# Kernel tuning notes

Hardware: AMD Instinct MI355X
Metric: run time of the kernel (lower is better)

## Reference

```python
import math
import jax, jax.numpy as jnp
import numpy as np

B, L, D, H = 256, 32, 512, 512
NEG_INF = -1e9


def setup_inputs() -> dict:
    key = jax.random.key(0)
    ks = jax.random.split(key, 7)
    x = jax.random.normal(ks[0], (B, L, D), dtype=jnp.float32)
    length = jax.random.randint(ks[1], (B,), 2, L + 1)  # valid lengths in [2, L]
    # word_linear: D -> 2H
    W_word = jax.random.normal(ks[2], (2 * H, D), dtype=jnp.float32) * (1.0 / math.sqrt(D))
    b_word = jnp.zeros((2 * H,), dtype=jnp.float32)
    # comp_linear: 2H -> 5H (orthogonal-ish init; scale is fine for a reference)
    W_comp = jax.random.normal(ks[3], (5 * H, 2 * H), dtype=jnp.float32) * (1.0 / math.sqrt(2 * H))
    b_comp = jnp.zeros((5 * H,), dtype=jnp.float32)
    comp_query = jax.random.normal(ks[4], (H,), dtype=jnp.float32) * 0.01
    return {"x": x, "length": length, "W_word": W_word, "b_word": b_word,
            "W_comp": W_comp, "b_comp": b_comp, "comp_query": comp_query}


def _treelstm_compose(hl, cl, hr, cr, W_comp, b_comp):
    # hl/hr: [B, n, H] -> parent h, c: [B, n, H]
    v = jnp.einsum('bnd,kd->bnk', jnp.concatenate([hl, hr], axis=2), W_comp) + b_comp
    i, fl, fr, u, o = jnp.split(v, 5, axis=2)
    c = cl * jax.nn.sigmoid(fl + 1.0) + cr * jax.nn.sigmoid(fr + 1.0) \
        + jnp.tanh(u) * jax.nn.sigmoid(i)
    h = jax.nn.sigmoid(o) * jnp.tanh(c)
    return h, c


def reference(x, length, W_word, b_word, W_comp, b_comp, comp_query):
    length_mask = (jnp.arange(L)[None, :] < length[:, None]).astype(jnp.float32)  # [B, L]
    # leaf states from word_linear (use_leaf_rnn=False path)
    hc = jnp.einsum('bld,kd->blk', x, W_word) + b_word  # [B, L, 2H]
    h, c = jnp.split(hc, 2, axis=2)
    scale = 1.0 / math.sqrt(H)
    for i in range(L - 1):
        new_h, new_c = _treelstm_compose(h[:, :-1], c[:, :-1], h[:, 1:], c[:, 1:], W_comp, b_comp)
        if i < L - 2:
            # eval-mode greedy composition selection (basic.greedy_select)
            logits = jnp.sum(comp_query * new_h, axis=-1) * scale  # [B, L-1-i]
            mask = length_mask[:, i + 1:]
            logits = jnp.where(mask > 0, logits, NEG_INF)
            select = jax.nn.one_hot(jnp.argmax(logits, axis=1), logits.shape[1], dtype=jnp.float32)
            cum = jnp.cumsum(select, axis=1)
            left = (1.0 - cum)[:, :, None]
            right = (cum - select)[:, :, None]
            sel = select[:, :, None]
            new_h = sel * new_h + left * h[:, :-1] + right * h[:, 1:]
            new_c = sel * new_c + left * c[:, :-1] + right * c[:, 1:]
        done = length_mask[:, i + 1][:, None, None]
        h = done * new_h + (1.0 - done) * h[:, :-1]
        c = done * new_c + (1.0 - done) * c[:, :-1]
    return h[:, 0, :]  # final root hidden state [B, H]
```

## Files before the change

### kernel.cpp

```cpp
#include <hip/hip_runtime.h>
#include <cmath>

#define B_   256
#define L_   32
#define H_   512
#define NH5  2560
#define N2   5120
#define SCALE 0.044194173824159216f

__device__ float g_h [B_*L_*H_];
__device__ float g_c [B_*L_*H_];
__device__ float g_al[(size_t)B_*L_*NH5];
__device__ float g_ar[(size_t)B_*L_*NH5];
__device__ float g_logit[B_*L_];
__device__ int   g_list[B_*L_];
__device__ int   g_count[B_];
__device__ int   g_merged[B_];
__device__ int   g_mpos[B_];
__device__ int   g_rows[B_*L_];
__device__ int   g_nrows;
__device__ int   g_mlist[2][B_];
__device__ int   g_cnt[2];

__device__ __forceinline__ float sigm(float x) { return 1.0f / (1.0f + expf(-x)); }

__device__ __forceinline__ void gate4(float* d, const float* __restrict__ a,
                                      const float* __restrict__ b,
                                      const float* __restrict__ bc, int off) {
  float4 x = *(const float4*)(a + off);
  float4 y = *(const float4*)(b + off);
  float4 z = *(const float4*)(bc + off);
  d[0]=x.x+y.x+z.x; d[1]=x.y+y.y+z.y; d[2]=x.z+y.z+z.z; d[3]=x.w+y.w+z.w;
}
__device__ __forceinline__ void gate2(float* d, const float* __restrict__ a,
                                      const float* __restrict__ b,
                                      const float* __restrict__ bc, int off) {
  float2 x = *(const float2*)(a + off);
  float2 y = *(const float2*)(b + off);
  float2 z = *(const float2*)(bc + off);
  d[0]=x.x+y.x+z.x; d[1]=x.y+y.y+z.y;
}

__global__ __launch_bounds__(256) void scan_init(const int* __restrict__ length) {
  __shared__ int sw[4];
  __shared__ int s_off[256];
  __shared__ int s_len[256];
  const int t = threadIdx.x;
  const int len = length[t];
  s_len[t] = len;
  int v = len;
#pragma unroll
  for (int off = 1; off < 64; off <<= 1) {
    int o = __shfl_up(v, off, 64);
    if ((t & 63) >= off) v += o;
  }
  if ((t & 63) == 63) sw[t >> 6] = v;
  __syncthreads();
  int base = 0;
  for (int w = 0; w < (t >> 6); w++) base += sw[w];
  const int incl = base + v;
  s_off[t] = incl - len;
  if (t == 255) g_nrows = incl;
  g_count[t] = len; g_merged[t] = -2; g_mpos[t] = 0;
  if (t == 0) { g_cnt[0] = 0; g_cnt[1] = 0; }
  __syncthreads();
  for (int idx = t; idx < B_*L_; idx += 256) {
    const int b = idx >> 5, s = idx & 31;
    g_list[idx] = s;
    if (s < s_len[b]) g_rows[s_off[b] + s] = idx;
  }
}

template<int MODE>
__global__ __launch_bounds__(512) void gemm_big(
    const float* __restrict__ Aext,
    const float* __restrict__ Bm,
    const float* __restrict__ bias)
{
  const int NR = g_nrows;
  const int m0 = blockIdx.y * 128;
  if (m0 >= NR) return;
  const int n0 = blockIdx.x * 128;

  const int tid = threadIdx.x;
  const int w = tid >> 6, l = tid & 63;
  const int tx = (w & 1) * 8 + (l & 7);
  const int ty = (w >> 1) * 8 + (l >> 3);

  __shared__ float As[8][128];
  __shared__ float Bs[8][128];

  const bool stgB = tid >= 256;
  const int st = tid & 255;
  const int rs = st >> 1, qs = (st & 1) * 4;

  const float* Abase = (MODE == 0) ? Aext : g_h;
  const float* sptr;
  if (!stgB) {
    int mr = m0 + rs; if (mr >= NR) mr = NR - 1;
    sptr = Abase + (size_t)g_rows[mr] * 512 + qs;
  } else {
    int nrow = n0 + rs;
    if (MODE == 0) sptr = Bm + (size_t)nrow * 512 + qs;
    else sptr = Bm + (nrow < NH5 ? (size_t)nrow * 1024
                                 : (size_t)(nrow - NH5) * 1024 + 512) + qs;
  }

  float4 sv = *(const float4*)(sptr);
  float acc[4][8] = {};

  for (int k0 = 0; k0 < 512; k0 += 8) {
    __syncthreads();
    if (!stgB) {
      As[qs+0][rs] = sv.x; As[qs+1][rs] = sv.y; As[qs+2][rs] = sv.z; As[qs+3][rs] = sv.w;
    } else {
      Bs[qs+0][rs] = sv.x; Bs[qs+1][rs] = sv.y; Bs[qs+2][rs] = sv.z; Bs[qs+3][rs] = sv.w;
    }
    __syncthreads();
    if (k0 + 8 < 512) sv = *(const float4*)(sptr + k0 + 8);
#pragma unroll
    for (int k = 0; k < 8; k++) {
      float4 a4 = *(const float4*)&As[k][ty*4];
      float af[4] = {a4.x, a4.y, a4.z, a4.w};
      float bf[8];
      float4 t0 = *(const float4*)&Bs[k][tx*8];
      float4 t1 = *(const float4*)&Bs[k][tx*8 + 4];
      bf[0]=t0.x; bf[1]=t0.y; bf[2]=t0.z; bf[3]=t0.w;
      bf[4]=t1.x; bf[5]=t1.y; bf[6]=t1.z; bf[7]=t1.w;
#pragma unroll
      for (int i = 0; i < 4; i++)
#pragma unroll
        for (int j = 0; j < 8; j++)
          acc[i][j] = fmaf(af[i], bf[j], acc[i][j]);
    }
  }

#pragma unroll
  for (int i = 0; i < 4; i++) {
    int mrow = m0 + ty*4 + i;
    if (mrow >= NR) continue;
    int crow = g_rows[mrow];
#pragma unroll
    for (int j = 0; j < 8; j++) {
      int n = n0 + tx*8 + j;
      float v = acc[i][j];
      if (MODE == 0) {
        v += bias[n];
        if (n < H_) g_h[(size_t)crow*H_ + n]        = v;
        else        g_c[(size_t)crow*H_ + (n - H_)] = v;
      } else {
        if (n < NH5) g_al[(size_t)crow*NH5 + n]         = v;
        else         g_ar[(size_t)crow*NH5 + (n - NH5)] = v;
      }
    }
  }
}

__global__ __launch_bounds__(256) void iter0_logits(const int* __restrict__ length,
                                                    const float* __restrict__ bc,
                                                    const float* __restrict__ qv) {
  __shared__ float sred[4];
  const int p = blockIdx.x, b = blockIdx.y;
  if (p >= length[b] - 1) return;
  const float* al = g_al + (size_t)(b*L_ + p)*NH5;
  const float* ar = g_ar + (size_t)(b*L_ + p + 1)*NH5;
  const float* cl = g_c  + (size_t)(b*L_ + p)*H_;
  const float* cr = g_c  + (size_t)(b*L_ + p + 1)*H_;
  const int j0 = threadIdx.x * 2;
  float vi[2], vfl[2], vfr[2], vu[2], vo[2];
  gate2(vi , al, ar, bc,        j0);
  gate2(vfl, al, ar, bc, H_   + j0);
  gate2(vfr, al, ar, bc, 2*H_ + j0);
  gate2(vu , al, ar, bc, 3*H_ + j0);
  gate2(vo , al, ar, bc, 4*H_ + j0);
  float2 CL = *(const float2*)(cl + j0);
  float2 CR = *(const float2*)(cr + j0);
  float2 Q  = *(const float2*)(qv + j0);
  const float clv[2] = {CL.x, CL.y};
  const float crv[2] = {CR.x, CR.y};
  const float qq [2] = {Q.x, Q.y};
  float part = 0.f;
#pragma unroll
  for (int u = 0; u < 2; ++u) {
    float c = clv[u]*sigm(vfl[u]+1.f) + crv[u]*sigm(vfr[u]+1.f) + tanhf(vu[u])*sigm(vi[u]);
    float h = sigm(vo[u])*tanhf(c);
    part = fmaf(qq[u], h, part);
  }
#pragma unroll
  for (int off = 32; off; off >>= 1) part += __shfl_down(part, off, 64);
  if ((threadIdx.x & 63) == 0) sred[threadIdx.x >> 6] = part;
  __syncthreads();
  if (threadIdx.x == 0)
    g_logit[b*L_ + p] = (sred[0]+sred[1]+sred[2]+sred[3]) * SCALE;
}

__global__ __launch_bounds__(512) void select_merge(int iter,
    const int* __restrict__ length,
    const float* __restrict__ bc,
    const float* __restrict__ qv,
    float* __restrict__ out)
{
  __shared__ float sred[4];
  __shared__ int s_sel[3];
  const int b = blockIdx.x, tid = threadIdx.x;
  const bool fin = (iter == L_-2);
  if (b == 0 && tid == 0) g_cnt[(iter & 1) ^ 1] = 0;

  const int m     = g_count[b];
  const int pslot = g_merged[b];
  const int ppos  = g_mpos[b];
  int* list = g_list + b*L_;

  if (iter > 0 && pslot >= 0) {
    const int half = tid >> 7, lt = tid & 127;
    int sl = -1, sr = -1;
    if (half == 0)      { if (ppos > 0)     { sl = list[ppos-1]; sr = list[ppos];   } }
    else if (half == 1) { if (ppos < m - 1) { sl = list[ppos];   sr = list[ppos+1]; } }
    float part = 0.f;
    if (sl >= 0) {
      const float* al = g_al + (size_t)(b*L_+sl)*NH5;
      const float* ar = g_ar + (size_t)(b*L_+sr)*NH5;
      const float* cl = g_c  + (size_t)(b*L_+sl)*H_;
      const float* cr = g_c  + (size_t)(b*L_+sr)*H_;
      const int j0 = lt * 4;
      float vi[4], vfl[4], vfr[4], vu[4], vo[4];
      gate4(vi , al, ar, bc,        j0);
      gate4(vfl, al, ar, bc, H_   + j0);
      gate4(vfr, al, ar, bc, 2*H_ + j0);
      gate4(vu , al, ar, bc, 3*H_ + j0);
      gate4(vo , al, ar, bc, 4*H_ + j0);
      float4 CL = *(const float4*)(cl + j0);
      float4 CR = *(const float4*)(cr + j0);
      float4 Q  = *(const float4*)(qv + j0);
      const float clv[4] = {CL.x,CL.y,CL.z,CL.w};
      const float crv[4] = {CR.x,CR.y,CR.z,CR.w};
      const float qq [4] = {Q.x,Q.y,Q.z,Q.w};
#pragma unroll
      for (int u = 0; u < 4; ++u) {
        float c = clv[u]*sigm(vfl[u]+1.f) + crv[u]*sigm(vfr[u]+1.f) + tanhf(vu[u])*sigm(vi[u]);
        float h = sigm(vo[u])*tanhf(c);
        part = fmaf(qq[u], h, part);
      }
    }
#pragma unroll
    for (int off = 32; off; off >>= 1) part += __shfl_down(part, off, 64);
    if ((tid & 63) == 0 && tid < 256) sred[tid >> 6] = part;
    __syncthreads();
    if (tid == 0   && ppos > 0)     g_logit[b*L_ + list[ppos-1]] = (sred[0]+sred[1])*SCALE;
    if (tid == 128 && ppos < m - 1) g_logit[b*L_ + list[ppos]]   = (sred[2]+sred[3])*SCALE;
  }

  const bool active = iter < (length[b] - 1);
  if (!active) {
    if (tid == 0) g_merged[b] = -1;
    if (fin)
      out[(size_t)b*H_ + tid] = g_h[(size_t)(b*L_)*H_ + tid];
    return;
  }

  __syncthreads();

  if (tid < 64) {
    float lg = -1e30f; int idx = tid;
    if (tid < m - 1) lg = g_logit[b*L_ + list[tid]];
#pragma unroll
    for (int off = 32; off; off >>= 1) {
      float olg = __shfl_down(lg, off, 64);
      int   oid = __shfl_down(idx, off, 64);
      if (olg > lg || (olg == lg && oid < idx)) { lg = olg; idx = oid; }
    }
    if (tid == 0) { s_sel[0] = idx; s_sel[1] = list[idx]; s_sel[2] = list[idx+1]; }
  }
  __syncthreads();
  const int pos = s_sel[0], sl = s_sel[1], sr = s_sel[2];

  {
    const float* al = g_al + (size_t)(b*L_+sl)*NH5;
    const float* ar = g_ar + (size_t)(b*L_+sr)*NH5;
    float*       cl = g_c  + (size_t)(b*L_+sl)*H_;
    const float* cr = g_c  + (size_t)(b*L_+sr)*H_;
    float*       hl = g_h  + (size_t)(b*L_+sl)*H_;
    const int j = tid;
    float vi  = al[j]       + ar[j]       + bc[j];
    float vfl = al[H_+j]    + ar[H_+j]    + bc[H_+j];
    float vfr = al[2*H_+j]  + ar[2*H_+j]  + bc[2*H_+j];
    float vu  = al[3*H_+j]  + ar[3*H_+j]  + bc[3*H_+j];
    float vo  = al[4*H_+j]  + ar[4*H_+j]  + bc[4*H_+j];
    float c = cl[j]*sigm(vfl+1.f) + cr[j]*sigm(vfr+1.f) + tanhf(vu)*sigm(vi);
    float h = sigm(vo)*tanhf(c);
    cl[j] = c; hl[j] = h;
    if (fin)
      out[(size_t)b*H_ + j] = h;
  }
  if (tid == 0) {
    for (int n = pos+1; n < m-1; n++) list[n] = list[n+1];
    g_count[b]  = m - 1;
    g_merged[b] = sl;
    g_mpos[b]   = pos;
    int k = atomicAdd(&g_cnt[iter & 1], 1);
    g_mlist[iter & 1][k] = b;
  }
}

__global__ __launch_bounds__(256) void gemm_iter(int par, const float* __restrict__ Wc)
{
  const int nact = g_cnt[par];
  const int m0 = blockIdx.y * 32;
  if (m0 >= nact) return;
  const int n0 = blockIdx.x * 64;
  const int tid = threadIdx.x;

  __shared__ float As[2][32][32];
  __shared__ float Bs[2][32][64];

  const int ra = tid >> 3, qa = (tid & 7) * 4;
  int mr = m0 + ra; if (mr >= nact) mr = nact - 1;
  const int bbA = g_mlist[par][mr];
  const float* aptr = g_h + (size_t)(bbA*L_ + g_merged[bbA]) * 512 + qa;

  const int rb = tid >> 2, qb = (tid & 3) * 8;
  const int nr = n0 + rb;
  const float* bptr = (nr < NH5) ? Wc + (size_t)nr * 1024 + qb
                                 : Wc + (size_t)(nr - NH5) * 1024 + 512 + qb;

  const int tx = tid & 15, ty = tid >> 4;

  float4 av  = *(const float4*)(aptr);
  float4 bv0 = *(const float4*)(bptr);
  float4 bv1 = *(const float4*)(bptr + 4);
  As[0][qa+0][ra]=av.x;  As[0][qa+1][ra]=av.y;  As[0][qa+2][ra]=av.z;  As[0][qa+3][ra]=av.w;
  Bs[0][qb+0][rb]=bv0.x; Bs[0][qb+1][rb]=bv0.y; Bs[0][qb+2][rb]=bv0.z; Bs[0][qb+3][rb]=bv0.w;
  Bs[0][qb+4][rb]=bv1.x; Bs[0][qb+5][rb]=bv1.y; Bs[0][qb+6][rb]=bv1.z; Bs[0][qb+7][rb]=bv1.w;
  __syncthreads();

  float acc[2][4] = {};
  for (int s = 0; s < 16; ++s) {
    const int cur = s & 1;
    if (s < 15) {
      const int ko = 32 * (s + 1);
      av  = *(const float4*)(aptr + ko);
      bv0 = *(const float4*)(bptr + ko);
      bv1 = *(const float4*)(bptr + ko + 4);
    }
#pragma unroll
    for (int k = 0; k < 32; k++) {
      float2 a2 = *(const float2*)&As[cur][k][ty*2];
      float4 b4 = *(const float4*)&Bs[cur][k][tx*4];
      acc[0][0] = fmaf(a2.x, b4.x, acc[0][0]);
      acc[0][1] = fmaf(a2.x, b4.y, acc[0][1]);
      acc[0][2] = fmaf(a2.x, b4.z, acc[0][2]);
      acc[0][3] = fmaf(a2.x, b4.w, acc[0][3]);
      acc[1][0] = fmaf(a2.y, b4.x, acc[1][0]);
      acc[1][1] = fmaf(a2.y, b4.y, acc[1][1]);
      acc[1][2] = fmaf(a2.y, b4.z, acc[1][2]);
      acc[1][3] = fmaf(a2.y, b4.w, acc[1][3]);
    }
    if (s < 15) {
      const int nx = cur ^ 1;
      As[nx][qa+0][ra]=av.x;  As[nx][qa+1][ra]=av.y;  As[nx][qa+2][ra]=av.z;  As[nx][qa+3][ra]=av.w;
      Bs[nx][qb+0][rb]=bv0.x; Bs[nx][qb+1][rb]=bv0.y; Bs[nx][qb+2][rb]=bv0.z; Bs[nx][qb+3][rb]=bv0.w;
      Bs[nx][qb+4][rb]=bv1.x; Bs[nx][qb+5][rb]=bv1.y; Bs[nx][qb+6][rb]=bv1.z; Bs[nx][qb+7][rb]=bv1.w;
      __syncthreads();
    }
  }

#pragma unroll
  for (int i = 0; i < 2; i++) {
    int mrow = m0 + ty*2 + i;
    if (mrow >= nact) continue;
    int bb = g_mlist[par][mrow];
    size_t base = (size_t)(bb*L_ + g_merged[bb]) * NH5;
    int n = n0 + tx*4;
    float4 v = make_float4(acc[i][0], acc[i][1], acc[i][2], acc[i][3]);
    if (n < NH5) *(float4*)(g_al + base + n)         = v;
    else         *(float4*)(g_ar + base + (n - NH5)) = v;
  }
}

extern "C" void kernel_launch(void* const* d_in, const int* in_sizes, int n_in,
                              void* d_out, int out_size, void* d_ws, size_t ws_size,
                              hipStream_t stream)
{
  (void)in_sizes; (void)n_in; (void)out_size; (void)d_ws; (void)ws_size;
  const float* x      = (const float*)d_in[0];
  const int*   length = (const int*)  d_in[1];
  const float* W_word = (const float*)d_in[2];
  const float* b_word = (const float*)d_in[3];
  const float* W_comp = (const float*)d_in[4];
  const float* b_comp = (const float*)d_in[5];
  const float* q      = (const float*)d_in[6];
  float* out = (float*)d_out;

  scan_init<<<1, 256, 0, stream>>>(length);

  gemm_big<0><<<dim3(1024/128, 64), 512, 0, stream>>>(x, W_word, b_word);
  gemm_big<1><<<dim3(N2/128,   64), 512, 0, stream>>>(nullptr, W_comp, nullptr);

  iter0_logits<<<dim3(L_-1, B_), 256, 0, stream>>>(length, b_comp, q);

  for (int i = 0; i < L_-1; i++) {
    select_merge<<<B_, 512, 0, stream>>>(i, length, b_comp, q, out);
    if (i < L_-2)
      gemm_iter<<<dim3(N2/64, 8), 256, 0, stream>>>(i & 1, W_comp);
  }
}
```

Before: 1.581 ms.

## Enlarge gemm_big per-thread tile and remap blocks to XCDs for weight locality

gemm_big drops from 512 to 256 threads per block, and each thread now computes an 8x8 output tile instead of 4x8, loading both A and B fragments itself. Both gemm_big and gemm_iter switch to a 1D grid whose block index is remapped so each of the 8 XCDs handles a fixed band of N tiles. This is meant to keep the weight columns resident in that XCD's L2 and to raise arithmetic intensity per thread. The cost is higher register pressure and fewer threads per block.

Result: no change. 1.570 ms (-0.7%).

```diff
diff --git a/kernel.cpp b/kernel.cpp
--- a/kernel.cpp
+++ b/kernel.cpp
@@ -72,15 +72,20 @@
 }
 
 template<int MODE>
-__global__ __launch_bounds__(512) void gemm_big(
+__global__ __launch_bounds__(256) void gemm_big(
     const float* __restrict__ Aext,
     const float* __restrict__ Bm,
     const float* __restrict__ bias)
 {
   const int NR = g_nrows;
-  const int m0 = blockIdx.y * 128;
+  const int bid = blockIdx.x;
+  const int xcd = bid & 7, jj = bid >> 3;
+  const int ntp = (MODE == 0) ? 1 : 5;
+  const int mt = jj / ntp;
+  const int nt = xcd * ntp + (jj - mt * ntp);
+  const int m0 = mt * 128;
   if (m0 >= NR) return;
-  const int n0 = blockIdx.x * 128;
+  const int n0 = nt * 128;
 
   const int tid = threadIdx.x;
   const int w = tid >> 6, l = tid & 63;
@@ -90,45 +95,48 @@
   __shared__ float As[8][128];
   __shared__ float Bs[8][128];
 
-  const bool stgB = tid >= 256;
-  const int st = tid & 255;
-  const int rs = st >> 1, qs = (st & 1) * 4;
+  const int ra = tid >> 1, qa = (tid & 1) * 4;
 
   const float* Abase = (MODE == 0) ? Aext : g_h;
-  const float* sptr;
-  if (!stgB) {
-    int mr = m0 + rs; if (mr >= NR) mr = NR - 1;
-    sptr = Abase + (size_t)g_rows[mr] * 512 + qs;
-  } else {
-    int nrow = n0 + rs;
-    if (MODE == 0) sptr = Bm + (size_t)nrow * 512 + qs;
-    else sptr = Bm + (nrow < NH5 ? (size_t)nrow * 1024
-                                 : (size_t)(nrow - NH5) * 1024 + 512) + qs;
-  }
-
-  float4 sv = *(const float4*)(sptr);
-  float acc[4][8] = {};
+  int mr = m0 + ra; if (mr >= NR) mr = NR - 1;
+  const float* aptr = Abase + (size_t)g_rows[mr] * 512 + qa;
+
+  const float* bptr;
+  {
+    int nrow = n0 + ra;
+    if (MODE == 0) bptr = Bm + (size_t)nrow * 512 + qa;
+    else bptr = Bm + (nrow < NH5 ? (size_t)nrow * 1024
+                                 : (size_t)(nrow - NH5) * 1024 + 512) + qa;
+  }
+
+  float4 av = *(const float4*)(aptr);
+  float4 bv = *(const float4*)(bptr);
+  float acc[8][8] = {};
 
   for (int k0 = 0; k0 < 512; k0 += 8) {
     __syncthreads();
-    if (!stgB) {
-      As[qs+0][rs] = sv.x; As[qs+1][rs] = sv.y; As[qs+2][rs] = sv.z; As[qs+3][rs] = sv.w;
-    } else {
-      Bs[qs+0][rs] = sv.x; Bs[qs+1][rs] = sv.y; Bs[qs+2][rs] = sv.z; Bs[qs+3][rs] = sv.w;
-    }
+    As[qa+0][ra] = av.x; As[qa+1][ra] = av.y; As[qa+2][ra] = av.z; As[qa+3][ra] = av.w;
+    Bs[qa+0][ra] = bv.x; Bs[qa+1][ra] = bv.y; Bs[qa+2][ra] = bv.z; Bs[qa+3][ra] = bv.w;
     __syncthreads();
-    if (k0 + 8 < 512) sv = *(const float4*)(sptr + k0 + 8);
+    if (k0 + 8 < 512) {
+      av = *(const float4*)(aptr + k0 + 8);
+      bv = *(const float4*)(bptr + k0 + 8);
+    }
 #pragma unroll
     for (int k = 0; k < 8; k++) {
-      float4 a4 = *(const float4*)&As[k][ty*4];
-      float af[4] = {a4.x, a4.y, a4.z, a4.w};
-      float bf[8];
-      float4 t0 = *(const float4*)&Bs[k][tx*8];
-      float4 t1 = *(const float4*)&Bs[k][tx*8 + 4];
-      bf[0]=t0.x; bf[1]=t0.y; bf[2]=t0.z; bf[3]=t0.w;
-      bf[4]=t1.x; bf[5]=t1.y; bf[6]=t1.z; bf[7]=t1.w;
-#pragma unroll
-      for (int i = 0; i < 4; i++)
+      float af[8], bf[8];
+#pragma unroll
+      for (int c = 0; c < 2; c++) {
+        float4 t = *(const float4*)&As[k][ty*8 + 4*c];
+        af[4*c+0]=t.x; af[4*c+1]=t.y; af[4*c+2]=t.z; af[4*c+3]=t.w;
+      }
+#pragma unroll
+      for (int c = 0; c < 2; c++) {
+        float4 t = *(const float4*)&Bs[k][tx*8 + 4*c];
+        bf[4*c+0]=t.x; bf[4*c+1]=t.y; bf[4*c+2]=t.z; bf[4*c+3]=t.w;
+      }
+#pragma unroll
+      for (int i = 0; i < 8; i++)
 #pragma unroll
         for (int j = 0; j < 8; j++)
           acc[i][j] = fmaf(af[i], bf[j], acc[i][j]);
@@ -136,8 +144,8 @@
   }
 
 #pragma unroll
-  for (int i = 0; i < 4; i++) {
-    int mrow = m0 + ty*4 + i;
+  for (int i = 0; i < 8; i++) {
+    int mrow = m0 + ty*8 + i;
     if (mrow >= NR) continue;
     int crow = g_rows[mrow];
 #pragma unroll
@@ -305,9 +313,13 @@
 __global__ __launch_bounds__(256) void gemm_iter(int par, const float* __restrict__ Wc)
 {
   const int nact = g_cnt[par];
-  const int m0 = blockIdx.y * 32;
+  const int bid = blockIdx.x;
+  const int xcd = bid & 7, jj = bid >> 3;
+  const int mt = jj / 10;
+  const int nt = xcd * 10 + (jj - mt * 10);
+  const int m0 = mt * 32;
   if (m0 >= nact) return;
-  const int n0 = blockIdx.x * 64;
+  const int n0 = nt * 64;
   const int tid = threadIdx.x;
 
   __shared__ float As[2][32][32];
@@ -393,14 +405,14 @@
 
   scan_init<<<1, 256, 0, stream>>>(length);
 
-  gemm_big<0><<<dim3(1024/128, 64), 512, 0, stream>>>(x, W_word, b_word);
-  gemm_big<1><<<dim3(N2/128,   64), 512, 0, stream>>>(nullptr, W_comp, nullptr);
+  gemm_big<0><<<8*64,  256, 0, stream>>>(x, W_word, b_word);
+  gemm_big<1><<<40*64, 256, 0, stream>>>(nullptr, W_comp, nullptr);
 
   iter0_logits<<<dim3(L_-1, B_), 256, 0, stream>>>(length, b_comp, q);
 
   for (int i = 0; i < L_-1; i++) {
     select_merge<<<B_, 512, 0, stream>>>(i, length, b_comp, q, out);
     if (i < L_-2)
-      gemm_iter<<<dim3(N2/64, 8), 256, 0, stream>>>(i & 1, W_comp);
-  }
-}
+      gemm_iter<<<640, 256, 0, stream>>>(i & 1, W_comp);
+  }
+}
```
